# Kernel tuning notes

Measured on AMD Instinct MI355X. Metric: run time of the kernel, lower is better.

The kernel has to match this reference:

```python
import jax, jax.numpy as jnp
import numpy as np

WS = 6      # window_size
SS = 3      # shift_size
NH = 8      # num_heads
DIM = 384
HD = DIM // NH
SCALE = HD ** -0.5


def _window_mask(H, W):
    # region ids: [:ss,:ss]=0, [:ss,ss:]=1, [ss:,:ss]=2, [ss:,ss:]=3
    row = (jnp.arange(H) >= SS).astype(jnp.int32)
    col = (jnp.arange(W) >= SS).astype(jnp.int32)
    region = row[:, None] * 2 + col[None, :]            # (H, W)
    region = jnp.roll(region, (-SS, -SS), axis=(0, 1))
    ids = region.reshape(H // WS, WS, W // WS, WS).transpose(0, 2, 1, 3)
    ids = ids.reshape(-1, WS * WS)                      # (nW, V)
    eq = ids[:, :, None] == ids[:, None, :]             # (nW, V, V)
    return jnp.where(eq, 0.0, -jnp.inf).astype(jnp.float32)


def setup_inputs():
    key = jax.random.key(0)
    k = jax.random.split(key, 5)
    B, H, W, D = 32, 48, 48, DIM
    return {
        "x": jax.random.normal(k[0], (B, H, W, D), jnp.float32),
        "w_qkv": jax.random.normal(k[1], (D, 3 * D), jnp.float32) * 0.02,
        "b_qkv": jax.random.normal(k[2], (3 * D,), jnp.float32) * 0.02,
        "w_proj": jax.random.normal(k[3], (D, D), jnp.float32) * 0.02,
        "b_proj": jax.random.normal(k[4], (D,), jnp.float32) * 0.02,
    }


def reference(x, w_qkv, b_qkv, w_proj, b_proj):
    B, H, W, D = x.shape
    nWh, nWw = H // WS, W // WS
    nW, V = nWh * nWw, WS * WS

    x = jnp.roll(x, (-SS, -SS), axis=(1, 2))
    amask = _window_mask(H, W)                          # (nW, V, V)

    # window partition -> (B*nW, V, D)
    xw = x.reshape(B, nWh, WS, nWw, WS, D).transpose(0, 1, 3, 2, 4, 5)
    xw = xw.reshape(B * nW, V, D)

    qkv = xw @ w_qkv + b_qkv                            # (M, V, 3D)
    qkv = qkv.reshape(B * nW, V, 3, NH, HD).transpose(2, 0, 3, 1, 4)
    q, k, v = qkv[0], qkv[1], qkv[2]                    # (M, NH, V, HD)

    scores = jnp.einsum("mhvd,mhud->mhvu", q, k) * SCALE
    scores = scores.reshape(B, nW, NH, V, V) + amask[None, :, None]
    attn = jax.nn.softmax(scores, axis=-1).reshape(B * nW, NH, V, V)

    out = jnp.einsum("mhvu,mhud->mhvd", attn, v)        # (M, NH, V, HD)
    out = out.transpose(0, 2, 1, 3).reshape(B * nW, V, D)

    # window reverse -> (B, H, W, D)
    out = out.reshape(B, nWh, nWw, WS, WS, D).transpose(0, 1, 3, 2, 4, 5)
    out = out.reshape(B, H, W, D)
    out = jnp.roll(out, (SS, SS), axis=(1, 2))
    return out @ w_proj + b_proj
```

## Files before the change

kernel.cpp:

```cpp
#include <hip/hip_runtime.h>
#include <hip/hip_bf16.h>

namespace {

constexpr int Bn   = 32;
constexpr int IMG  = 48;
constexpr int Dm   = 384;
constexpr int NHn  = 8;
constexpr int WSn  = 6;
constexpr int NWn  = 64;
constexpr int Mn   = Bn * NWn;
constexpr int Vn   = 36;
constexpr int ROWS = Mn * Vn;
constexpr int K3   = 3 * Dm;
constexpr int HEADS_E = Vn * 48;
constexpr float SCALE = 0.14433756729740643f;

using short8 = __attribute__((ext_vector_type(8))) short;
using f32x4  = __attribute__((ext_vector_type(4))) float;

__device__ __forceinline__ float bf2f(unsigned short u) {
    return __uint_as_float(((unsigned)u) << 16);
}
__device__ __forceinline__ unsigned short f2bf(float f) {
    unsigned u = __float_as_uint(f);
    u += 0x7FFFu + ((u >> 16) & 1u);
    return (unsigned short)(u >> 16);
}

__device__ __forceinline__ void gl_lds16(const unsigned short* g, unsigned short* l) {
    __builtin_amdgcn_global_load_lds(
        (const __attribute__((address_space(1))) unsigned int*)g,
        (__attribute__((address_space(3))) unsigned int*)l, 16, 0, 0);
}

__device__ __forceinline__ int gather_base(int row) {
    int m = row / Vn, v = row - m * Vn;
    int b = m >> 6, w = m & 63;
    int wh = w >> 3, ww = w & 7;
    int gh = wh * WSn + v / WSn;
    int gw = ww * WSn + v % WSn;
    int fi = (gh + 3) % IMG;
    int fj = (gw + 3) % IMG;
    return ((b * IMG + fi) * IMG + fj) * Dm;
}

__device__ __forceinline__ int region_id(int t, int wh, int ww) {
    int hi = (wh == 7) ? ((t / 6) < 3) : 1;
    int lo = (ww == 7) ? ((t % 6) < 3) : 1;
    return (hi << 1) | lo;
}

__global__ __launch_bounds__(256)
void gather_x(const float* __restrict__ x, unsigned short* __restrict__ xg)
{
    int idx = blockIdx.x * 256 + threadIdx.x;
    int row = idx / 96;
    int c4  = (idx - row * 96) * 4;
    float4 v = *(const float4*)(x + (size_t)gather_base(row) + c4);
    ushort4 o;
    o.x = f2bf(v.x); o.y = f2bf(v.y); o.z = f2bf(v.z); o.w = f2bf(v.w);
    *(ushort4*)(xg + (size_t)row * Dm + c4) = o;
}

__global__ __launch_bounds__(256)
void prep_w(const float* __restrict__ wq, const float* __restrict__ wp,
            unsigned short* __restrict__ wqT, unsigned short* __restrict__ wpT)
{
    int idx = blockIdx.x * 256 + threadIdx.x;
    if (idx < K3 * Dm) {
        int n = idx / Dm, k = idx - n * Dm;
        wqT[idx] = f2bf(wq[(size_t)k * K3 + n]);
    } else {
        int i2 = idx - K3 * Dm;
        if (i2 < Dm * Dm) {
            int n = i2 / Dm, k = i2 - n * Dm;
            wpT[i2] = f2bf(wp[(size_t)k * Dm + n]);
        }
    }
}

__global__ __launch_bounds__(256)
void qkv_mfma(const unsigned short* __restrict__ xg,
              const unsigned short* __restrict__ wqT,
              const float* __restrict__ bq,
              unsigned short* __restrict__ qh,
              unsigned short* __restrict__ kh,
              unsigned short* __restrict__ vh)
{
    __shared__ __align__(16) unsigned short As[128 * 32];
    __shared__ __align__(16) unsigned short Bs[128 * 32];

    const int tid  = threadIdx.x;
    const int wave = tid >> 6, lane = tid & 63;
    const int quad = lane >> 4, l15 = lane & 15;
    const int id = (blockIdx.x & 7) * 648 + (blockIdx.x >> 3);
    const int nT = id % (K3 / 128);
    const int mT = id / (K3 / 128);
    const int rowA0 = mT * 128, rowB0 = nT * 128;

    const int r_in = lane >> 2;
    const int kc   = (lane & 3) * 8;
    const unsigned short* gA = xg  + (size_t)(rowA0 + wave * 32 + r_in) * Dm + kc;
    const unsigned short* gB = wqT + (size_t)(rowB0 + wave * 32 + r_in) * Dm + kc;
    unsigned short* lA0 = &As[(wave * 32) * 32];
    unsigned short* lA1 = &As[(wave * 32 + 16) * 32];
    unsigned short* lB0 = &Bs[(wave * 32) * 32];
    unsigned short* lB1 = &Bs[(wave * 32 + 16) * 32];

    const int wm = wave >> 1, wn = wave & 1;
    f32x4 acc[4][4];
#pragma unroll
    for (int i = 0; i < 4; i++)
#pragma unroll
        for (int j = 0; j < 4; j++) acc[i][j] = (f32x4){0.f, 0.f, 0.f, 0.f};

    for (int k0 = 0; k0 < Dm; k0 += 32) {
        __syncthreads();
        gl_lds16(gA + k0, lA0);
        gl_lds16(gA + 16 * Dm + k0, lA1);
        gl_lds16(gB + k0, lB0);
        gl_lds16(gB + 16 * Dm + k0, lB1);
        __syncthreads();
        short8 af[4], bf[4];
#pragma unroll
        for (int i = 0; i < 4; i++)
            af[i] = *(const short8*)&As[(wm * 64 + i * 16 + l15) * 32 + quad * 8];
#pragma unroll
        for (int j = 0; j < 4; j++)
            bf[j] = *(const short8*)&Bs[(wn * 64 + j * 16 + l15) * 32 + quad * 8];
#pragma unroll
        for (int i = 0; i < 4; i++)
#pragma unroll
            for (int j = 0; j < 4; j++)
                acc[i][j] = __builtin_amdgcn_mfma_f32_16x16x32_bf16(af[i], bf[j], acc[i][j], 0, 0, 0);
    }

    unsigned short* outb = (nT < 3) ? qh : (nT < 6) ? kh : vh;
    const int csub = (nT < 3) ? 0 : (nT < 6) ? 384 : 768;
#pragma unroll
    for (int j = 0; j < 4; j++) {
        int col = rowB0 + wn * 64 + j * 16 + l15;
        float b = bq[col];
        int c  = col - csub;
        int hh = c / 48, dd = c - hh * 48;
#pragma unroll
        for (int i = 0; i < 4; i++) {
#pragma unroll
            for (int r = 0; r < 4; r++) {
                int row = rowA0 + wm * 64 + i * 16 + quad * 4 + r;
                int mm = row / 36, vv = row - mm * 36;
                outb[((size_t)(mm * 8 + hh) * 36 + vv) * 48 + dd] = f2bf(acc[i][j][r] + b);
            }
        }
    }
}

__global__ __launch_bounds__(256)
void attn_mfma(const unsigned short* __restrict__ qh,
               const unsigned short* __restrict__ kh,
               const unsigned short* __restrict__ vh,
               unsigned short* __restrict__ att)
{
    __shared__ __align__(16) unsigned short Pl[4][48 * 56];
    __shared__ __align__(16) unsigned short Vt[4][48 * 64];

    const int tid  = threadIdx.x;
    const int wave = tid >> 6, lane = tid & 63;
    const int quad = lane >> 4, l15 = lane & 15;
    const int W = blockIdx.x * 4 + wave;
    const int m = W >> 3, h = W & 7;
    const int w = m & 63, wh = w >> 3, ww = w & 7;
    const bool need_mask = (wh == 7) || (ww == 7);

    const short8 zf = {0, 0, 0, 0, 0, 0, 0, 0};

    {
        short8* vz = (short8*)&Vt[0][0];
#pragma unroll
        for (int z = 0; z < 6; z++) vz[z * 256 + tid] = zf;
    }
    __syncthreads();

    const size_t hb = (size_t)(m * 8 + h) * HEADS_E;

    const unsigned short* qb = qh + hb;
    const unsigned short* kb = kh + hb;
    short8 qf[3][2], kf[3][2];
#pragma unroll
    for (int t = 0; t < 3; t++) {
        const unsigned short* qr = qb + (t * 16 + l15) * 48;
        qf[t][0] = *(const short8*)(qr + quad * 8);
        qf[t][1] = (quad < 2) ? *(const short8*)(qr + 32 + quad * 8) : zf;
        const unsigned short* kr = kb + (t * 16 + l15) * 48;
        kf[t][0] = *(const short8*)(kr + quad * 8);
        kf[t][1] = *(const short8*)(kr + 32 + quad * 8);
    }

    unsigned short* vws = &Vt[wave][0];
    {
        const unsigned short* vb = vh + hb;
#pragma unroll
        for (int p = 0; p < 4; p++) {
            int c = p * 64 + lane;
            if (c < 216) {
                short8 vv = *(const short8*)(vb + c * 8);
                int v  = c / 6, d0 = (c - v * 6) * 8;
                int g  = v >> 3, v7 = v & 7;
#pragma unroll
                for (int jj = 0; jj < 8; jj++) {
                    int d = d0 + jj;
                    int slot = (g + (d & 7) + (d >> 3)) & 7;
                    vws[d * 64 + slot * 8 + v7] = (unsigned short)vv[jj];
                }
            }
        }
    }

    f32x4 acc[3][3];
#pragma unroll
    for (int i = 0; i < 3; i++)
#pragma unroll
        for (int j = 0; j < 3; j++) acc[i][j] = (f32x4){0.f, 0.f, 0.f, 0.f};
    __builtin_amdgcn_s_setprio(1);
#pragma unroll
    for (int i = 0; i < 3; i++)
#pragma unroll
        for (int j = 0; j < 3; j++) {
            acc[i][j] = __builtin_amdgcn_mfma_f32_16x16x32_bf16(qf[i][0], kf[j][0], acc[i][j], 0, 0, 0);
            acc[i][j] = __builtin_amdgcn_mfma_f32_16x16x32_bf16(qf[i][1], kf[j][1], acc[i][j], 0, 0, 0);
        }
    __builtin_amdgcn_s_setprio(0);

#pragma unroll
    for (int i = 0; i < 3; i++) {
        float rs[4] = {0.f, 0.f, 0.f, 0.f};
        if (need_mask) {
#pragma unroll
            for (int j = 0; j < 3; j++) {
                int C = j * 16 + l15;
                int idc = region_id(C, wh, ww);
#pragma unroll
                for (int r = 0; r < 4; r++) {
                    int R = i * 16 + quad * 4 + r;
                    int idr = region_id(R, wh, ww);
                    float s = acc[i][j][r] * SCALE;
                    s = (C >= 36 || idr != idc) ? -1e30f : fminf(s, 30.f);
                    float e = __expf(s);
                    acc[i][j][r] = e;
                    rs[r] += e;
                }
            }
        } else {
#pragma unroll
            for (int j = 0; j < 3; j++) {
                int C = j * 16 + l15;
#pragma unroll
                for (int r = 0; r < 4; r++) {
                    float s = acc[i][j][r] * SCALE;
                    s = (C >= 36) ? -1e30f : fminf(s, 30.f);
                    float e = __expf(s);
                    acc[i][j][r] = e;
                    rs[r] += e;
                }
            }
        }
#pragma unroll
        for (int r = 0; r < 4; r++) {
#pragma unroll
            for (int d = 1; d < 16; d <<= 1) rs[r] += __shfl_xor(rs[r], d, 16);
            rs[r] = 1.f / rs[r];
        }
#pragma unroll
        for (int j = 0; j < 3; j++)
#pragma unroll
            for (int r = 0; r < 4; r++) {
                int R = i * 16 + quad * 4 + r;
                int C = j * 16 + l15;
                Pl[wave][R * 56 + C] = f2bf(acc[i][j][r] * rs[r]);
            }
    }
    __syncthreads();

    short8 pf[3][2], vf[3][2];
#pragma unroll
    for (int t = 0; t < 3; t++) {
        const unsigned short* pr = &Pl[wave][(t * 16 + l15) * 56];
        pf[t][0] = *(const short8*)(pr + quad * 8);
        pf[t][1] = (quad < 2) ? *(const short8*)(pr + 32 + quad * 8) : zf;
        int d  = t * 16 + l15;
        int sb = (d & 7) + (d >> 3);
        vf[t][0] = *(const short8*)(vws + d * 64 + (((quad + sb) & 7) * 8));
        vf[t][1] = *(const short8*)(vws + d * 64 + (((quad + 4 + sb) & 7) * 8));
    }
    f32x4 oacc[3][3];
#pragma unroll
    for (int i = 0; i < 3; i++)
#pragma unroll
        for (int j = 0; j < 3; j++) oacc[i][j] = (f32x4){0.f, 0.f, 0.f, 0.f};
    __builtin_amdgcn_s_setprio(1);
#pragma unroll
    for (int i = 0; i < 3; i++)
#pragma unroll
        for (int j = 0; j < 3; j++) {
            oacc[i][j] = __builtin_amdgcn_mfma_f32_16x16x32_bf16(pf[i][0], vf[j][0], oacc[i][j], 0, 0, 0);
            oacc[i][j] = __builtin_amdgcn_mfma_f32_16x16x32_bf16(pf[i][1], vf[j][1], oacc[i][j], 0, 0, 0);
        }
    __builtin_amdgcn_s_setprio(0);

#pragma unroll
    for (int i = 0; i < 3; i++)
#pragma unroll
        for (int r = 0; r < 4; r++) {
            int R = i * 16 + quad * 4 + r;
            if (R < 36) {
#pragma unroll
                for (int j = 0; j < 3; j++)
                    att[((size_t)m * 36 + R) * Dm + h * 48 + j * 16 + l15] = f2bf(oacc[i][j][r]);
            }
        }
}

__global__ __launch_bounds__(256)
void proj_mfma(const unsigned short* __restrict__ att,
               const unsigned short* __restrict__ wpT,
               const float* __restrict__ bp,
               float* __restrict__ out)
{
    __shared__ __align__(16) unsigned short As[128 * 32];
    __shared__ __align__(16) unsigned short Bs[128 * 32];
    __shared__ int rowOut[128];

    const int tid  = threadIdx.x;
    const int wave = tid >> 6, lane = tid & 63;
    const int quad = lane >> 4, l15 = lane & 15;
    const int id = (blockIdx.x & 7) * 216 + (blockIdx.x >> 3);
    const int nT = id % (Dm / 128);
    const int mT = id / (Dm / 128);
    const int rowA0 = mT * 128, rowB0 = nT * 128;

    if (tid < 128) rowOut[tid] = gather_base(rowA0 + tid);

    const int r_in = lane >> 2;
    const int kc   = (lane & 3) * 8;
    const unsigned short* gA = att + (size_t)(rowA0 + wave * 32 + r_in) * Dm + kc;
    const unsigned short* gB = wpT + (size_t)(rowB0 + wave * 32 + r_in) * Dm + kc;
    unsigned short* lA0 = &As[(wave * 32) * 32];
    unsigned short* lA1 = &As[(wave * 32 + 16) * 32];
    unsigned short* lB0 = &Bs[(wave * 32) * 32];
    unsigned short* lB1 = &Bs[(wave * 32 + 16) * 32];

    const int wm = wave >> 1, wn = wave & 1;
    f32x4 acc[4][4];
#pragma unroll
    for (int i = 0; i < 4; i++)
#pragma unroll
        for (int j = 0; j < 4; j++) acc[i][j] = (f32x4){0.f, 0.f, 0.f, 0.f};

    for (int k0 = 0; k0 < Dm; k0 += 32) {
        __syncthreads();
        gl_lds16(gA + k0, lA0);
        gl_lds16(gA + 16 * Dm + k0, lA1);
        gl_lds16(gB + k0, lB0);
        gl_lds16(gB + 16 * Dm + k0, lB1);
        __syncthreads();
        short8 af[4], bf[4];
#pragma unroll
        for (int i = 0; i < 4; i++)
            af[i] = *(const short8*)&As[(wm * 64 + i * 16 + l15) * 32 + quad * 8];
#pragma unroll
        for (int j = 0; j < 4; j++)
            bf[j] = *(const short8*)&Bs[(wn * 64 + j * 16 + l15) * 32 + quad * 8];
#pragma unroll
        for (int i = 0; i < 4; i++)
#pragma unroll
            for (int j = 0; j < 4; j++)
                acc[i][j] = __builtin_amdgcn_mfma_f32_16x16x32_bf16(af[i], bf[j], acc[i][j], 0, 0, 0);
    }

#pragma unroll
    for (int j = 0; j < 4; j++) {
        int col = rowB0 + wn * 64 + j * 16 + l15;
        float b = bp[col];
#pragma unroll
        for (int i = 0; i < 4; i++) {
#pragma unroll
            for (int r = 0; r < 4; r++) {
                int lrow = wm * 64 + i * 16 + quad * 4 + r;
                out[(size_t)rowOut[lrow] + col] = acc[i][j][r] + b;
            }
        }
    }
}

}

extern "C" void kernel_launch(void* const* d_in, const int* in_sizes, int n_in,
                              void* d_out, int out_size, void* d_ws, size_t ws_size,
                              hipStream_t stream)
{
    const float* x  = (const float*)d_in[0];
    const float* wq = (const float*)d_in[1];
    const float* bq = (const float*)d_in[2];
    const float* wp = (const float*)d_in[3];
    const float* bp = (const float*)d_in[4];
    float* out = (float*)d_out;

    const size_t HE   = (size_t)Mn * NHn * HEADS_E;
    const size_t XG_E = (size_t)ROWS * Dm;
    unsigned short* qh  = (unsigned short*)d_ws;
    unsigned short* kh  = qh + HE;
    unsigned short* vh  = kh + HE;
    unsigned short* xg  = vh + HE;
    unsigned short* att = xg;
    unsigned short* wqT = xg + XG_E;
    unsigned short* wpT = wqT + (size_t)K3 * Dm;

    prep_w   <<<(K3 * Dm + Dm * Dm + 255) / 256, 256, 0, stream>>>(wq, wp, wqT, wpT);
    gather_x <<<ROWS * (Dm / 4) / 256,            256, 0, stream>>>(x, xg);
    qkv_mfma <<<(ROWS / 128) * (K3 / 128),        256, 0, stream>>>(xg, wqT, bq, qh, kh, vh);
    attn_mfma<<<(Mn * NHn) / 4,                   256, 0, stream>>>(qh, kh, vh, att);
    proj_mfma<<<(ROWS / 128) * (Dm / 128),        256, 0, stream>>>(att, wpT, bp, out);
}
```

Baseline: 411.6 us.

## Fuse window gather and bf16 cast into QKV GEMM, swizzle LDS layout

Removes the separate gather_x kernel. The QKV GEMM now reads fp32 x directly at the shifted-window addresses, converts it to bf16 in registers, and stores it into LDS, with the next k-slice prefetched into registers. Both GEMMs also use an XOR-swizzled LDS layout (invol) to cut bank conflicts on the MFMA fragment reads. This saves one kernel launch and the bf16 intermediate round-trip. In exchange, the QKV kernel reads x once per N-tile (9 times) in fp32 and does conversion work inside the GEMM loop.

```diff
diff --git a/kernel.cpp b/kernel.cpp
--- a/kernel.cpp
+++ b/kernel.cpp
@@ -28,6 +28,10 @@
     return (unsigned short)(u >> 16);
 }
 
+__device__ __forceinline__ int invol(int f) {
+    return (f & 56) | ((f ^ (f >> 3)) & 7);
+}
+
 __device__ __forceinline__ void gl_lds16(const unsigned short* g, unsigned short* l) {
     __builtin_amdgcn_global_load_lds(
         (const __attribute__((address_space(1))) unsigned int*)g,
@@ -49,18 +53,6 @@
     int hi = (wh == 7) ? ((t / 6) < 3) : 1;
     int lo = (ww == 7) ? ((t % 6) < 3) : 1;
     return (hi << 1) | lo;
-}
-
-__global__ __launch_bounds__(256)
-void gather_x(const float* __restrict__ x, unsigned short* __restrict__ xg)
-{
-    int idx = blockIdx.x * 256 + threadIdx.x;
-    int row = idx / 96;
-    int c4  = (idx - row * 96) * 4;
-    float4 v = *(const float4*)(x + (size_t)gather_base(row) + c4);
-    ushort4 o;
-    o.x = f2bf(v.x); o.y = f2bf(v.y); o.z = f2bf(v.z); o.w = f2bf(v.w);
-    *(ushort4*)(xg + (size_t)row * Dm + c4) = o;
 }
 
 __global__ __launch_bounds__(256)
@@ -81,7 +73,7 @@
 }
 
 __global__ __launch_bounds__(256)
-void qkv_mfma(const unsigned short* __restrict__ xg,
+void qkv_mfma(const float* __restrict__ x,
               const unsigned short* __restrict__ wqT,
               const float* __restrict__ bq,
               unsigned short* __restrict__ qh,
@@ -99,41 +91,77 @@
     const int mT = id / (K3 / 128);
     const int rowA0 = mT * 128, rowB0 = nT * 128;
 
-    const int r_in = lane >> 2;
-    const int kc   = (lane & 3) * 8;
-    const unsigned short* gA = xg  + (size_t)(rowA0 + wave * 32 + r_in) * Dm + kc;
-    const unsigned short* gB = wqT + (size_t)(rowB0 + wave * 32 + r_in) * Dm + kc;
-    unsigned short* lA0 = &As[(wave * 32) * 32];
-    unsigned short* lA1 = &As[(wave * 32 + 16) * 32];
+    const int r32 = lane >> 1;
+    const int hc  = lane & 1;
+    const float* gsrc = x + (size_t)gather_base(rowA0 + wave * 32 + r32) + hc * 16;
+    const int fA0 = (r32 & 15) * 4 + hc * 2;
+    unsigned short* wAb = &As[wave * 1024 + (r32 >> 4) * 512];
+    unsigned short* wA0 = wAb + invol(fA0) * 8;
+    unsigned short* wA1 = wAb + invol(fA0 + 1) * 8;
+
+    const int fB   = invol(lane);
+    const int rB   = fB >> 2;
+    const int kcB  = (fB & 3) * 8;
+    const unsigned short* gB = wqT + (size_t)(rowB0 + wave * 32 + rB) * Dm + kcB;
     unsigned short* lB0 = &Bs[(wave * 32) * 32];
     unsigned short* lB1 = &Bs[(wave * 32 + 16) * 32];
 
     const int wm = wave >> 1, wn = wave & 1;
+    int aoff[4], boff[4];
+#pragma unroll
+    for (int i = 0; i < 4; i++) {
+        int R = wm * 64 + i * 16 + l15;
+        aoff[i] = (R >> 4) * 512 + invol((R & 15) * 4 + quad) * 8;
+        int S = wn * 64 + i * 16 + l15;
+        boff[i] = (S >> 4) * 512 + invol((S & 15) * 4 + quad) * 8;
+    }
+
     f32x4 acc[4][4];
 #pragma unroll
     for (int i = 0; i < 4; i++)
 #pragma unroll
         for (int j = 0; j < 4; j++) acc[i][j] = (f32x4){0.f, 0.f, 0.f, 0.f};
+
+    float4 fA[4];
+#pragma unroll
+    for (int u = 0; u < 4; u++) fA[u] = *(const float4*)(gsrc + u * 4);
 
     for (int k0 = 0; k0 < Dm; k0 += 32) {
         __syncthreads();
-        gl_lds16(gA + k0, lA0);
-        gl_lds16(gA + 16 * Dm + k0, lA1);
         gl_lds16(gB + k0, lB0);
         gl_lds16(gB + 16 * Dm + k0, lB1);
+        {
+            short8 w0, w1;
+#pragma unroll
+            for (int u = 0; u < 2; u++) {
+                w0[u * 4 + 0] = (short)f2bf(fA[u].x);
+                w0[u * 4 + 1] = (short)f2bf(fA[u].y);
+                w0[u * 4 + 2] = (short)f2bf(fA[u].z);
+                w0[u * 4 + 3] = (short)f2bf(fA[u].w);
+                w1[u * 4 + 0] = (short)f2bf(fA[u + 2].x);
+                w1[u * 4 + 1] = (short)f2bf(fA[u + 2].y);
+                w1[u * 4 + 2] = (short)f2bf(fA[u + 2].z);
+                w1[u * 4 + 3] = (short)f2bf(fA[u + 2].w);
+            }
+            *(short8*)wA0 = w0;
+            *(short8*)wA1 = w1;
+        }
         __syncthreads();
-        short8 af[4], bf[4];
+        if (k0 + 32 < Dm) {
+#pragma unroll
+            for (int u = 0; u < 4; u++)
+                fA[u] = *(const float4*)(gsrc + (k0 + 32) + u * 4);
+        }
+        short8 af[4], bfr[4];
+#pragma unroll
+        for (int i = 0; i < 4; i++) af[i]  = *(const short8*)&As[aoff[i]];
+#pragma unroll
+        for (int j = 0; j < 4; j++) bfr[j] = *(const short8*)&Bs[boff[j]];
 #pragma unroll
         for (int i = 0; i < 4; i++)
-            af[i] = *(const short8*)&As[(wm * 64 + i * 16 + l15) * 32 + quad * 8];
-#pragma unroll
-        for (int j = 0; j < 4; j++)
-            bf[j] = *(const short8*)&Bs[(wn * 64 + j * 16 + l15) * 32 + quad * 8];
-#pragma unroll
-        for (int i = 0; i < 4; i++)
 #pragma unroll
             for (int j = 0; j < 4; j++)
-                acc[i][j] = __builtin_amdgcn_mfma_f32_16x16x32_bf16(af[i], bf[j], acc[i][j], 0, 0, 0);
+                acc[i][j] = __builtin_amdgcn_mfma_f32_16x16x32_bf16(af[i], bfr[j], acc[i][j], 0, 0, 0);
     }
 
     unsigned short* outb = (nT < 3) ? qh : (nT < 6) ? kh : vh;
@@ -341,16 +369,26 @@
 
     if (tid < 128) rowOut[tid] = gather_base(rowA0 + tid);
 
-    const int r_in = lane >> 2;
-    const int kc   = (lane & 3) * 8;
-    const unsigned short* gA = att + (size_t)(rowA0 + wave * 32 + r_in) * Dm + kc;
-    const unsigned short* gB = wpT + (size_t)(rowB0 + wave * 32 + r_in) * Dm + kc;
+    const int fP  = invol(lane);
+    const int rIn = fP >> 2;
+    const int kc  = (fP & 3) * 8;
+    const unsigned short* gA = att + (size_t)(rowA0 + wave * 32 + rIn) * Dm + kc;
+    const unsigned short* gB = wpT + (size_t)(rowB0 + wave * 32 + rIn) * Dm + kc;
     unsigned short* lA0 = &As[(wave * 32) * 32];
     unsigned short* lA1 = &As[(wave * 32 + 16) * 32];
     unsigned short* lB0 = &Bs[(wave * 32) * 32];
     unsigned short* lB1 = &Bs[(wave * 32 + 16) * 32];
 
     const int wm = wave >> 1, wn = wave & 1;
+    int aoff[4], boff[4];
+#pragma unroll
+    for (int i = 0; i < 4; i++) {
+        int R = wm * 64 + i * 16 + l15;
+        aoff[i] = (R >> 4) * 512 + invol((R & 15) * 4 + quad) * 8;
+        int S = wn * 64 + i * 16 + l15;
+        boff[i] = (S >> 4) * 512 + invol((S & 15) * 4 + quad) * 8;
+    }
+
     f32x4 acc[4][4];
 #pragma unroll
     for (int i = 0; i < 4; i++)
@@ -364,18 +402,16 @@
         gl_lds16(gB + k0, lB0);
         gl_lds16(gB + 16 * Dm + k0, lB1);
         __syncthreads();
-        short8 af[4], bf[4];
+        short8 af[4], bfr[4];
+#pragma unroll
+        for (int i = 0; i < 4; i++) af[i]  = *(const short8*)&As[aoff[i]];
+#pragma unroll
+        for (int j = 0; j < 4; j++) bfr[j] = *(const short8*)&Bs[boff[j]];
 #pragma unroll
         for (int i = 0; i < 4; i++)
-            af[i] = *(const short8*)&As[(wm * 64 + i * 16 + l15) * 32 + quad * 8];
-#pragma unroll
-        for (int j = 0; j < 4; j++)
-            bf[j] = *(const short8*)&Bs[(wn * 64 + j * 16 + l15) * 32 + quad * 8];
-#pragma unroll
-        for (int i = 0; i < 4; i++)
 #pragma unroll
             for (int j = 0; j < 4; j++)
-                acc[i][j] = __builtin_amdgcn_mfma_f32_16x16x32_bf16(af[i], bf[j], acc[i][j], 0, 0, 0);
+                acc[i][j] = __builtin_amdgcn_mfma_f32_16x16x32_bf16(af[i], bfr[j], acc[i][j], 0, 0, 0);
     }
 
 #pragma unroll
@@ -411,14 +447,12 @@
     unsigned short* qh  = (unsigned short*)d_ws;
     unsigned short* kh  = qh + HE;
     unsigned short* vh  = kh + HE;
-    unsigned short* xg  = vh + HE;
-    unsigned short* att = xg;
-    unsigned short* wqT = xg + XG_E;
+    unsigned short* att = vh + HE;
+    unsigned short* wqT = att + XG_E;
     unsigned short* wpT = wqT + (size_t)K3 * Dm;
 
     prep_w   <<<(K3 * Dm + Dm * Dm + 255) / 256, 256, 0, stream>>>(wq, wp, wqT, wpT);
-    gather_x <<<ROWS * (Dm / 4) / 256,            256, 0, stream>>>(x, xg);
-    qkv_mfma <<<(ROWS / 128) * (K3 / 128),        256, 0, stream>>>(xg, wqT, bq, qh, kh, vh);
+    qkv_mfma <<<(ROWS / 128) * (K3 / 128),        256, 0, stream>>>(x, wqT, bq, qh, kh, vh);
     attn_mfma<<<(Mn * NHn) / 4,                   256, 0, stream>>>(qh, kh, vh, att);
     proj_mfma<<<(ROWS / 128) * (Dm / 128),        256, 0, stream>>>(att, wpT, bp, out);
 }
```

Measured after the change: 448.3 us. 8.9% more time.

## Double-buffer LDS staging and XOR-swizzle layout in QKV and projection GEMMs

Applied to the files above, without the earlier changes.

Both MFMA GEMM kernels now use two LDS buffers. The next K-slice is issued with global_load_lds while MFMAs run on the current one, and each iteration needs one barrier instead of two. The LDS layout is also XOR-swizzled through an involution of the lane index, applied both to which global chunk each lane loads and to the read offsets, to cut bank conflicts on the short8 reads. The cost is double the LDS footprint, which may reduce occupancy. The prefetch relies on the barrier at the end of the previous iteration to guard the buffer it overwrites.

```diff
diff --git a/kernel.cpp b/kernel.cpp
--- a/kernel.cpp
+++ b/kernel.cpp
@@ -28,6 +28,10 @@
     return (unsigned short)(u >> 16);
 }
 
+__device__ __forceinline__ int invol(int f) {
+    return (f & 56) | ((f ^ (f >> 3)) & 7);
+}
+
 __device__ __forceinline__ void gl_lds16(const unsigned short* g, unsigned short* l) {
     __builtin_amdgcn_global_load_lds(
         (const __attribute__((address_space(1))) unsigned int*)g,
@@ -88,8 +92,8 @@
               unsigned short* __restrict__ kh,
               unsigned short* __restrict__ vh)
 {
-    __shared__ __align__(16) unsigned short As[128 * 32];
-    __shared__ __align__(16) unsigned short Bs[128 * 32];
+    __shared__ __align__(16) unsigned short As[2][128 * 32];
+    __shared__ __align__(16) unsigned short Bs[2][128 * 32];
 
     const int tid  = threadIdx.x;
     const int wave = tid >> 6, lane = tid & 63;
@@ -99,41 +103,52 @@
     const int mT = id / (K3 / 128);
     const int rowA0 = mT * 128, rowB0 = nT * 128;
 
-    const int r_in = lane >> 2;
-    const int kc   = (lane & 3) * 8;
-    const unsigned short* gA = xg  + (size_t)(rowA0 + wave * 32 + r_in) * Dm + kc;
-    const unsigned short* gB = wqT + (size_t)(rowB0 + wave * 32 + r_in) * Dm + kc;
-    unsigned short* lA0 = &As[(wave * 32) * 32];
-    unsigned short* lA1 = &As[(wave * 32 + 16) * 32];
-    unsigned short* lB0 = &Bs[(wave * 32) * 32];
-    unsigned short* lB1 = &Bs[(wave * 32 + 16) * 32];
+    const int fS  = invol(lane);
+    const int rS  = fS >> 2;
+    const int kcS = (fS & 3) * 8;
+    const unsigned short* gA = xg  + (size_t)(rowA0 + wave * 32 + rS) * Dm + kcS;
+    const unsigned short* gB = wqT + (size_t)(rowB0 + wave * 32 + rS) * Dm + kcS;
 
     const int wm = wave >> 1, wn = wave & 1;
+    int aoff[4], boff[4];
+#pragma unroll
+    for (int i = 0; i < 4; i++) {
+        int R = wm * 64 + i * 16 + l15;
+        aoff[i] = (R >> 4) * 512 + invol((R & 15) * 4 + quad) * 8;
+        int S = wn * 64 + i * 16 + l15;
+        boff[i] = (S >> 4) * 512 + invol((S & 15) * 4 + quad) * 8;
+    }
+
+    auto STAGE = [&](int buf, int k0) {
+        gl_lds16(gA + k0,           &As[buf][(wave * 32) * 32]);
+        gl_lds16(gA + 16 * Dm + k0, &As[buf][(wave * 32 + 16) * 32]);
+        gl_lds16(gB + k0,           &Bs[buf][(wave * 32) * 32]);
+        gl_lds16(gB + 16 * Dm + k0, &Bs[buf][(wave * 32 + 16) * 32]);
+    };
+
     f32x4 acc[4][4];
 #pragma unroll
     for (int i = 0; i < 4; i++)
 #pragma unroll
         for (int j = 0; j < 4; j++) acc[i][j] = (f32x4){0.f, 0.f, 0.f, 0.f};
 
+    STAGE(0, 0);
+    __syncthreads();
+
     for (int k0 = 0; k0 < Dm; k0 += 32) {
-        __syncthreads();
-        gl_lds16(gA + k0, lA0);
-        gl_lds16(gA + 16 * Dm + k0, lA1);
-        gl_lds16(gB + k0, lB0);
-        gl_lds16(gB + 16 * Dm + k0, lB1);
-        __syncthreads();
-        short8 af[4], bf[4];
+        const int cur = (k0 >> 5) & 1;
+        if (k0 + 32 < Dm) STAGE(cur ^ 1, k0 + 32);
+        short8 af[4], bfr[4];
+#pragma unroll
+        for (int i = 0; i < 4; i++) af[i]  = *(const short8*)&As[cur][aoff[i]];
+#pragma unroll
+        for (int j = 0; j < 4; j++) bfr[j] = *(const short8*)&Bs[cur][boff[j]];
 #pragma unroll
         for (int i = 0; i < 4; i++)
-            af[i] = *(const short8*)&As[(wm * 64 + i * 16 + l15) * 32 + quad * 8];
-#pragma unroll
-        for (int j = 0; j < 4; j++)
-            bf[j] = *(const short8*)&Bs[(wn * 64 + j * 16 + l15) * 32 + quad * 8];
-#pragma unroll
-        for (int i = 0; i < 4; i++)
 #pragma unroll
             for (int j = 0; j < 4; j++)
-                acc[i][j] = __builtin_amdgcn_mfma_f32_16x16x32_bf16(af[i], bf[j], acc[i][j], 0, 0, 0);
+                acc[i][j] = __builtin_amdgcn_mfma_f32_16x16x32_bf16(af[i], bfr[j], acc[i][j], 0, 0, 0);
+        if (k0 + 32 < Dm) __syncthreads();
     }
 
     unsigned short* outb = (nT < 3) ? qh : (nT < 6) ? kh : vh;
@@ -327,8 +342,8 @@
                const float* __restrict__ bp,
                float* __restrict__ out)
 {
-    __shared__ __align__(16) unsigned short As[128 * 32];
-    __shared__ __align__(16) unsigned short Bs[128 * 32];
+    __shared__ __align__(16) unsigned short As[2][128 * 32];
+    __shared__ __align__(16) unsigned short Bs[2][128 * 32];
     __shared__ int rowOut[128];
 
     const int tid  = threadIdx.x;
@@ -341,41 +356,52 @@
 
     if (tid < 128) rowOut[tid] = gather_base(rowA0 + tid);
 
-    const int r_in = lane >> 2;
-    const int kc   = (lane & 3) * 8;
-    const unsigned short* gA = att + (size_t)(rowA0 + wave * 32 + r_in) * Dm + kc;
-    const unsigned short* gB = wpT + (size_t)(rowB0 + wave * 32 + r_in) * Dm + kc;
-    unsigned short* lA0 = &As[(wave * 32) * 32];
-    unsigned short* lA1 = &As[(wave * 32 + 16) * 32];
-    unsigned short* lB0 = &Bs[(wave * 32) * 32];
-    unsigned short* lB1 = &Bs[(wave * 32 + 16) * 32];
+    const int fS  = invol(lane);
+    const int rS  = fS >> 2;
+    const int kcS = (fS & 3) * 8;
+    const unsigned short* gA = att + (size_t)(rowA0 + wave * 32 + rS) * Dm + kcS;
+    const unsigned short* gB = wpT + (size_t)(rowB0 + wave * 32 + rS) * Dm + kcS;
 
     const int wm = wave >> 1, wn = wave & 1;
+    int aoff[4], boff[4];
+#pragma unroll
+    for (int i = 0; i < 4; i++) {
+        int R = wm * 64 + i * 16 + l15;
+        aoff[i] = (R >> 4) * 512 + invol((R & 15) * 4 + quad) * 8;
+        int S = wn * 64 + i * 16 + l15;
+        boff[i] = (S >> 4) * 512 + invol((S & 15) * 4 + quad) * 8;
+    }
+
+    auto STAGE = [&](int buf, int k0) {
+        gl_lds16(gA + k0,           &As[buf][(wave * 32) * 32]);
+        gl_lds16(gA + 16 * Dm + k0, &As[buf][(wave * 32 + 16) * 32]);
+        gl_lds16(gB + k0,           &Bs[buf][(wave * 32) * 32]);
+        gl_lds16(gB + 16 * Dm + k0, &Bs[buf][(wave * 32 + 16) * 32]);
+    };
+
     f32x4 acc[4][4];
 #pragma unroll
     for (int i = 0; i < 4; i++)
 #pragma unroll
         for (int j = 0; j < 4; j++) acc[i][j] = (f32x4){0.f, 0.f, 0.f, 0.f};
 
+    STAGE(0, 0);
+    __syncthreads();
+
     for (int k0 = 0; k0 < Dm; k0 += 32) {
-        __syncthreads();
-        gl_lds16(gA + k0, lA0);
-        gl_lds16(gA + 16 * Dm + k0, lA1);
-        gl_lds16(gB + k0, lB0);
-        gl_lds16(gB + 16 * Dm + k0, lB1);
-        __syncthreads();
-        short8 af[4], bf[4];
+        const int cur = (k0 >> 5) & 1;
+        if (k0 + 32 < Dm) STAGE(cur ^ 1, k0 + 32);
+        short8 af[4], bfr[4];
+#pragma unroll
+        for (int i = 0; i < 4; i++) af[i]  = *(const short8*)&As[cur][aoff[i]];
+#pragma unroll
+        for (int j = 0; j < 4; j++) bfr[j] = *(const short8*)&Bs[cur][boff[j]];
 #pragma unroll
         for (int i = 0; i < 4; i++)
-            af[i] = *(const short8*)&As[(wm * 64 + i * 16 + l15) * 32 + quad * 8];
-#pragma unroll
-        for (int j = 0; j < 4; j++)
-            bf[j] = *(const short8*)&Bs[(wn * 64 + j * 16 + l15) * 32 + quad * 8];
-#pragma unroll
-        for (int i = 0; i < 4; i++)
 #pragma unroll
             for (int j = 0; j < 4; j++)
-                acc[i][j] = __builtin_amdgcn_mfma_f32_16x16x32_bf16(af[i], bf[j], acc[i][j], 0, 0, 0);
+                acc[i][j] = __builtin_amdgcn_mfma_f32_16x16x32_bf16(af[i], bfr[j], acc[i][j], 0, 0, 0);
+        if (k0 + 32 < Dm) __syncthreads();
     }
 
 #pragma unroll
```

Result: slower. 421.3 us (+2.4%).
